# Optimization experiments

Hardware: AMD Instinct MI355X
Metric: run time of the kernel (lower is better)

The kernel has to match this reference:

```python
import jax, jax.numpy as jnp
import numpy as np

B, C, H, W = 8, 1024, 56, 56
NBINS = 256          # torch.histc(bins=256, min=0, max=1)
T_THRESH = 0.9       # EKLM entropy-ratio threshold
NUM_CLASSES = 30


def setup_inputs() -> dict:
    key = jax.random.key(0)
    k1, k2 = jax.random.split(key)
    x = jax.random.uniform(k1, (B, C, H, W), dtype=jnp.float32)
    w_fc = jax.random.normal(k2, (C, NUM_CLASSES), dtype=jnp.float32) * 0.02
    return {"x": x, "w_fc": w_fc}


def _integral_hist(x):
    """One fused pass replacing the per-region torch.histc calls.
    Returns per-(h,w)-cell histograms [H,W,256] and their 2D inclusive
    prefix sum padded to [H+1,W+1,256] so any rectangle histogram is 4 lookups.
    Matches torch.histc semantics: values outside [0,1] ignored, v==1 -> last bin."""
    valid = (x >= 0.0) & (x <= 1.0)
    q = jnp.clip(jnp.floor(x * NBINS), 0, NBINS - 1).astype(jnp.int32)
    q = jnp.where(valid, q, NBINS)  # out-of-range -> extra bin, dropped below
    hh = jnp.broadcast_to(jnp.arange(H)[None, None, :, None], x.shape)
    ww = jnp.broadcast_to(jnp.arange(W)[None, None, None, :], x.shape)
    cell = jnp.zeros((H, W, NBINS + 1), jnp.float32).at[hh, ww, q].add(1.0)[..., :NBINS]
    integ = jnp.cumsum(jnp.cumsum(cell, axis=0), axis=1)
    integ = jnp.pad(integ, ((1, 0), (1, 0), (0, 0)))  # [H+1, W+1, 256]
    return cell, integ


def _entropy_of_hist(h):
    p = h / jnp.sum(h)
    return -jnp.sum(p * jnp.log2(p + 1e-9))


def _region_entropy(integ, xs, xd, ys, yd):
    # histogram of x[:, :, xs:xd, ys:yd] via integral-histogram lookups
    h = integ[xd, yd] - integ[xs, yd] - integ[xd, ys] + integ[xs, ys]
    return _entropy_of_hist(h)


def eklm(x):
    """Entropy-based Key Localization Method (xs fixed to 0, as in source)."""
    cell, integ = _integral_hist(x)
    # compute_entropy_for_each_y: entropy of each [:, :, 0:1, y:y+1] column cell
    col_hists = cell[0]  # [W, 256]
    p = col_hists / jnp.sum(col_hists, axis=1, keepdims=True)
    ent_y = -jnp.sum(p * jnp.log2(p + 1e-9), axis=1)
    ys0 = jnp.argmax(ent_y).astype(jnp.int32)
    total_ent = _region_entropy(integ, 0, H, 0, W)

    def ent(xd, ys, yd):
        return _region_entropy(integ, 0, xd, ys, yd)

    def cond(state):
        xd, ys, yd, Ts, done = state
        return (Ts < T_THRESH) & (~done)

    def body(state):
        xd, ys, yd, Ts, done = state
        e_cur = ent(xd, ys, yd)
        # greedy priority identical to source: grow xd, else shrink ys, else grow yd
        c1 = (xd + 1 < H) & (ent(xd + 1, ys, yd) > e_cur)
        c2 = (~c1) & (ys - 1 >= 0) & (ent(xd, jnp.maximum(ys - 1, 0), yd) > e_cur)
        c3 = (~c1) & (~c2) & (yd + 1 < W) & (ent(xd, ys, jnp.minimum(yd + 1, W)) > e_cur)
        xd_n = jnp.where(c1, xd + 1, xd)
        ys_n = jnp.where(c2, ys - 1, ys)
        yd_n = jnp.where(c3, yd + 1, yd)
        done_n = ~(c1 | c2 | c3)
        Ts_n = ent(xd_n, ys_n, yd_n) / total_ent
        return (xd_n, ys_n, yd_n, Ts_n, done_n)

    xd0 = jnp.int32(1)
    yd0 = ys0 + jnp.int32(1)
    Ts0 = ent(xd0, ys0, yd0) / total_ent
    xd, ys, yd, _, _ = jax.lax.while_loop(
        cond, body, (xd0, ys0, yd0, Ts0, jnp.bool_(False)))
    return jnp.int32(0), xd, ys, yd


def reference(x, w_fc):
    xs, xd, ys, yd = eklm(x)
    # crop the located key region (mask form for static shapes), mean-pool, classify
    row = jnp.arange(H)
    col = jnp.arange(W)
    mask = ((row[:, None] >= xs) & (row[:, None] < xd)
            & (col[None, :] >= ys) & (col[None, :] < yd)).astype(x.dtype)
    area = jnp.maximum(jnp.sum(mask), 1.0)
    pooled = jnp.einsum('bchw,hw->bc', x, mask) / area  # [B, C]
    return pooled @ w_fc  # [B, NUM_CLASSES]
```

## Files before the change

kernel.cpp:

```cpp
#include <hip/hip_runtime.h>
#include <math.h>

#define BB 8
#define CC 1024
#define HH 56
#define WW 56
#define NB 256
#define NCLS 30
#define BC (BB * CC)
#define PLANE (HH * WW)
#define NWORD (NB / 2)
#define CELLW (PLANE * NWORD)
#define SLICES 16
#define PL_PER_SLICE (BC / SLICES)

#define NPART 16
#define GH_BLOCKS 3136
#define F4_PER_BLOCK 2048
#define FB_BLOCKS 256

#define FULL_NEED 28934400ull
#define META_OFF 28901376ull

__global__ void zero_kernel(unsigned* __restrict__ p, unsigned* __restrict__ bar) {
    p[blockIdx.x * 256 + threadIdx.x] = 0u;
    if (blockIdx.x == 0 && threadIdx.x < 8) bar[threadIdx.x] = 0u;
}

__global__ __launch_bounds__(256) void ghist_kernel(const float* __restrict__ x,
                                                    unsigned* __restrict__ colhist,
                                                    unsigned* __restrict__ gpart) {
    __shared__ unsigned lh[4 * NB];
    const int tid = threadIdx.x;
    lh[tid] = 0u; lh[NB + tid] = 0u; lh[2 * NB + tid] = 0u; lh[3 * NB + tid] = 0u;
    __syncthreads();

    const size_t base_f4 = (size_t)blockIdx.x * F4_PER_BLOCK;
    const float4* __restrict__ xb = (const float4*)x + base_f4;
    float4 v[8];
#pragma unroll
    for (int it = 0; it < 8; ++it) v[it] = xb[it * 256 + tid];

    unsigned* wl = lh + ((tid >> 6) << 8);
#pragma unroll
    for (int it = 0; it < 8; ++it) {
        const int j = it * 256 + tid;
        const int e0 = ((int)base_f4 + j) * 4;
        const int pl = e0 / PLANE;
        const int li = e0 - pl * PLANE;
        const bool r0 = (li < WW);
        const float vv[4] = {v[it].x, v[it].y, v[it].z, v[it].w};
#pragma unroll
        for (int e = 0; e < 4; ++e) {
            const float f = vv[e];
            if (f >= 0.f && f <= 1.f) {
                int bin = (int)(f * 256.f);
                if (bin > 255) bin = 255;
                atomicAdd(&wl[bin], 1u);
                if (r0) atomicAdd(&colhist[(li + e) * NB + bin], 1u);
            }
        }
    }
    __syncthreads();
    const unsigned s = lh[tid] + lh[NB + tid] + lh[2 * NB + tid] + lh[3 * NB + tid];
    if (s) atomicAdd(&gpart[((blockIdx.x & (NPART - 1)) << 8) + tid], s);
}

__device__ __forceinline__ float wave_sum(float v) {
#pragma unroll
    for (int off = 32; off > 0; off >>= 1) v += __shfl_xor(v, off);
    return v;
}

__device__ __forceinline__ float ilook(const unsigned* __restrict__ integ,
                                       int a, int b, int bin) {
    return (a == 0 || b == 0)
               ? 0.f
               : (float)integ[((size_t)((a - 1) * WW + (b - 1))) * NB + bin];
}

__device__ float region_ent(const unsigned* __restrict__ integ, int lane,
                            int xd, int ys, int yd) {
    float hb[4];
    float hs = 0.f;
#pragma unroll
    for (int k = 0; k < 4; k++) {
        const int bin = lane + 64 * k;
        const float hv = ilook(integ, xd, yd, bin) - ilook(integ, xd, ys, bin);
        hb[k] = hv;
        hs += hv;
    }
    hs = wave_sum(hs);
    float e = 0.f;
#pragma unroll
    for (int k = 0; k < 4; k++) {
        const float p = hb[k] / hs;
        e += p * log2f(p + 1e-9f);
    }
    return -wave_sum(e);
}

__global__ __launch_bounds__(1024) void decide_fast_kernel(
    const unsigned* __restrict__ colhist, const unsigned* __restrict__ gpart,
    int* __restrict__ region, unsigned* __restrict__ flag) {
    __shared__ float ent_s[WW];
    const int tid = threadIdx.x;
    const int lane = tid & 63;
    const int wv = tid >> 6;

    for (int w = wv; w < WW; w += 16) {
        float hb[4], hs = 0.f;
#pragma unroll
        for (int k = 0; k < 4; k++) {
            const int bin = lane + 64 * k;
            hb[k] = (float)colhist[w * NB + bin];
            hs += hb[k];
        }
        hs = wave_sum(hs);
        float e = 0.f;
#pragma unroll
        for (int k = 0; k < 4; k++) {
            const float p = hb[k] / hs;
            e += p * log2f(p + 1e-9f);
        }
        e = -wave_sum(e);
        if (lane == 0) ent_s[w] = e;
    }
    __syncthreads();
    if (wv != 0) return;

    float best = -3.0e38f;
    int bestw = 0;
    for (int w = 0; w < WW; ++w) {
        const float e = ent_s[w];
        if (e > best) { best = e; bestw = w; }
    }

    float hb[4], hs = 0.f;
#pragma unroll
    for (int k = 0; k < 4; k++) {
        const int bin = lane + 64 * k;
        unsigned t = 0;
#pragma unroll
        for (int p = 0; p < NPART; ++p) t += gpart[(p << 8) + bin];
        hb[k] = (float)t;
        hs += hb[k];
    }
    hs = wave_sum(hs);
    float e = 0.f;
#pragma unroll
    for (int k = 0; k < 4; k++) {
        const float p = hb[k] / hs;
        e += p * log2f(p + 1e-9f);
    }
    const float total_ent = -wave_sum(e);

    const float Ts0 = best / total_ent;
    if (lane == 0) {
        region[0] = 1;
        region[1] = bestw;
        region[2] = bestw + 1;
        *flag = (Ts0 >= 0.9f) ? 1u : 2u;
    }
}

__device__ __forceinline__ void soft_grid_sync(unsigned* __restrict__ bar,
                                               int idx, unsigned nb) {
    __syncthreads();
    if (threadIdx.x == 0) {
        __threadfence();
        atomicAdd(&bar[idx], 1u);
        while (atomicAdd(&bar[idx], 0u) < nb) {
            __builtin_amdgcn_s_sleep(8);
        }
    }
    __syncthreads();
    __threadfence();
}

__global__ __launch_bounds__(256) void fallback_kernel(
    const float* __restrict__ x, unsigned* __restrict__ ps,
    unsigned* __restrict__ hist, int* __restrict__ region,
    const unsigned* __restrict__ flag, unsigned* __restrict__ bar) {
    if (*flag == 1u) return;
    __shared__ unsigned lh[HH * NWORD];
    const int tid = threadIdx.x;
    const int gtid = blockIdx.x * 256 + tid;

    for (int t = blockIdx.x; t < HH * SLICES; t += FB_BLOCKS) {
        const int h = t % HH;
        const int slice = t / HH;
        for (int i = tid; i < HH * NWORD; i += 256) lh[i] = 0u;
        __syncthreads();
        const float* __restrict__ xb =
            x + (size_t)(slice * PL_PER_SLICE) * PLANE + h * WW;
        for (int it = 0; it < 28; ++it) {
            const int j = it * 256 + tid;
            const int bcl = j / 14;
            const int wq = j - bcl * 14;
            const float4 v = *(const float4*)(xb + (size_t)bcl * PLANE + wq * 4);
            const float vv[4] = {v.x, v.y, v.z, v.w};
#pragma unroll
            for (int e = 0; e < 4; ++e) {
                const float f = vv[e];
                if (f >= 0.f && f <= 1.f) {
                    int bin = (int)(f * 256.f);
                    if (bin > 255) bin = 255;
                    atomicAdd(&lh[(wq * 4 + e) * NWORD + (bin >> 1)],
                              1u << ((bin & 1) << 4));
                }
            }
        }
        __syncthreads();
        unsigned* g = ps + (size_t)slice * CELLW + (size_t)h * WW * NWORD;
        for (int i = tid; i < HH * NWORD; i += 256) g[i] = lh[i];
        __syncthreads();
    }
    soft_grid_sync(bar, 0, FB_BLOCKS);

    for (int idx = gtid; idx < CELLW; idx += FB_BLOCKS * 256) {
        unsigned s = 0;
#pragma unroll
        for (int sl = 0; sl < SLICES; ++sl) s += ps[(size_t)sl * CELLW + idx];
        ((uint2*)hist)[idx] = make_uint2(s & 0xffffu, s >> 16);
    }
    soft_grid_sync(bar, 1, FB_BLOCKS);

    if (gtid < HH * NB) {
        const int h = gtid >> 8, b = gtid & 255;
        unsigned* base = hist + (size_t)h * WW * NB + b;
        unsigned v[WW];
#pragma unroll
        for (int w = 0; w < WW; ++w) v[w] = base[(size_t)w * NB];
        unsigned c = 0;
#pragma unroll
        for (int w = 0; w < WW; ++w) { c += v[w]; base[(size_t)w * NB] = c; }
    }
    soft_grid_sync(bar, 2, FB_BLOCKS);

    if (gtid < WW * NB) {
        const int w = gtid >> 8, b = gtid & 255;
        unsigned* base = hist + (size_t)w * NB + b;
        unsigned v[HH];
#pragma unroll
        for (int h = 0; h < HH; ++h) v[h] = base[(size_t)h * WW * NB];
        unsigned c = 0;
#pragma unroll
        for (int h = 0; h < HH; ++h) { c += v[h]; base[(size_t)h * WW * NB] = c; }
    }
    soft_grid_sync(bar, 3, FB_BLOCKS);

    if (blockIdx.x == 0 && tid < 64) {
        const int lane = tid;
        const float total_ent = region_ent(hist, lane, HH, 0, WW);
        int xd = region[0], ys = region[1], yd = region[2];
        float Ts = region_ent(hist, lane, xd, ys, yd) / total_ent;
        bool done = false;
        int iter = 0;
        while (Ts < 0.9f && !done && iter < 1000) {
            iter++;
            const float e_cur = region_ent(hist, lane, xd, ys, yd);
            const int ysm = (ys - 1 < 0) ? 0 : ys - 1;
            const int ydp = (yd + 1 > WW) ? WW : yd + 1;
            const bool c1 = (xd + 1 < HH) &&
                            (region_ent(hist, lane, xd + 1, ys, yd) > e_cur);
            const bool c2 = !c1 && (ys - 1 >= 0) &&
                            (region_ent(hist, lane, xd, ysm, yd) > e_cur);
            const bool c3 = !c1 && !c2 && (yd + 1 < WW) &&
                            (region_ent(hist, lane, xd, ys, ydp) > e_cur);
            if (c1) xd = xd + 1;
            else if (c2) ys = ys - 1;
            else if (c3) yd = yd + 1;
            done = !(c1 || c2 || c3);
            Ts = region_ent(hist, lane, xd, ys, yd) / total_ent;
        }
        if (lane == 0) {
            region[0] = xd;
            region[1] = ys;
            region[2] = yd;
        }
    }
}

__global__ __launch_bounds__(256) void fc_kernel(const float* __restrict__ x,
                                                 const int* __restrict__ region,
                                                 const float* __restrict__ wfc,
                                                 float* __restrict__ out) {
    __shared__ float pl_s[CC];
    __shared__ float red[240];
    const int b = blockIdx.x;
    const int t = threadIdx.x;
    const int xd = region[0], ys = region[1], yd = region[2];
    const int Wd = yd - ys;
    const int n = xd * Wd;
    const float area = fmaxf((float)n, 1.f);
    const float* __restrict__ xb = x + (size_t)b * CC * PLANE;
#pragma unroll
    for (int k = 0; k < 4; ++k) {
        const int c = t + k * 256;
        const float* plane = xb + (size_t)c * PLANE;
        float s = 0.f;
        for (int j = 0; j < n; ++j) {
            const int r = j / Wd;
            const int cc2 = ys + (j - r * Wd);
            s += plane[r * WW + cc2];
        }
        pl_s[c] = s / area;
    }
    __syncthreads();
    if (t < 240) {
        const int chunk = t / NCLS;
        const int nn = t - chunk * NCLS;
        const float* pv = pl_s + chunk * 128;
        const float* wv = wfc + (size_t)(chunk * 128) * NCLS + nn;
        float a0 = 0.f, a1 = 0.f, a2 = 0.f, a3 = 0.f;
        for (int c = 0; c < 128; c += 4) {
            a0 += pv[c + 0] * wv[(c + 0) * NCLS];
            a1 += pv[c + 1] * wv[(c + 1) * NCLS];
            a2 += pv[c + 2] * wv[(c + 2) * NCLS];
            a3 += pv[c + 3] * wv[(c + 3) * NCLS];
        }
        red[t] = (a0 + a1) + (a2 + a3);
    }
    __syncthreads();
    if (t < NCLS) {
        float s = 0.f;
#pragma unroll
        for (int ch = 0; ch < 8; ++ch) s += red[ch * NCLS + t];
        out[b * NCLS + t] = s;
    }
}

extern "C" void kernel_launch(void* const* d_in, const int* in_sizes, int n_in,
                              void* d_out, int out_size, void* d_ws, size_t ws_size,
                              hipStream_t stream) {
    const float* x = (const float*)d_in[0];
    const float* wfc = (const float*)d_in[1];
    float* out = (float*)d_out;

    unsigned char* ws = (unsigned char*)d_ws;
    const bool full = (ws_size >= FULL_NEED);

    unsigned* colhist = (unsigned*)ws;
    unsigned* gpart = (unsigned*)(ws + 57344);
    unsigned* ps = (unsigned*)ws;
    unsigned* hist = (unsigned*)(ws + (size_t)SLICES * CELLW * 4);
    int* region;
    unsigned* flag;
    unsigned* bar;
    if (full) {
        unsigned char* meta = ws + META_OFF;
        region = (int*)meta;
        flag = (unsigned*)(meta + 16);
        bar = (unsigned*)(meta + 32);
    } else {
        region = (int*)(ws + 73728);
        flag = (unsigned*)(ws + 73728 + 16);
        bar = (unsigned*)(ws + 73728 + 32);
    }

    zero_kernel<<<72, 256, 0, stream>>>(colhist, bar);
    ghist_kernel<<<GH_BLOCKS, 256, 0, stream>>>(x, colhist, gpart);
    decide_fast_kernel<<<1, 1024, 0, stream>>>(colhist, gpart, region, flag);
    if (full) {
        fallback_kernel<<<FB_BLOCKS, 256, 0, stream>>>(x, ps, hist, region,
                                                       flag, bar);
    }
    fc_kernel<<<BB, 256, 0, stream>>>(x, region, wfc, out);
}
```

Baseline: 169.8 us.

## Fuse histogram, decision, fallback and FC into one persistent kernel

Merges the global-histogram, decision, fallback integral-histogram and FC kernels into a single persistent 1024-block kernel that uses hierarchical software grid barriers between phases. Column histograms are now accumulated in packed 16-bit shared-memory counters per block and flushed once, instead of global atomics per element. The fallback path is rewritten to build cell histograms with global atomics directly, replacing the sliced partial buffers. This removes several kernel launches and intermediate round trips. In exchange it relies on all 1024 blocks being co-resident, and the fc phase runs on only 8 blocks at the end.

```diff
diff --git a/kernel.cpp b/kernel.cpp
--- a/kernel.cpp
+++ b/kernel.cpp
@@ -10,60 +10,40 @@
 #define BC (BB * CC)
 #define PLANE (HH * WW)
 #define NWORD (NB / 2)
-#define CELLW (PLANE * NWORD)
-#define SLICES 16
-#define PL_PER_SLICE (BC / SLICES)
-
+#define CHW (HH * NWORD)
 #define NPART 16
-#define GH_BLOCKS 3136
-#define F4_PER_BLOCK 2048
-#define FB_BLOCKS 256
-
-#define FULL_NEED 28934400ull
-#define META_OFF 28901376ull
-
-__global__ void zero_kernel(unsigned* __restrict__ p, unsigned* __restrict__ bar) {
-    p[blockIdx.x * 256 + threadIdx.x] = 0u;
-    if (blockIdx.x == 0 && threadIdx.x < 8) bar[threadIdx.x] = 0u;
-}
-
-__global__ __launch_bounds__(256) void ghist_kernel(const float* __restrict__ x,
-                                                    unsigned* __restrict__ colhist,
-                                                    unsigned* __restrict__ gpart) {
-    __shared__ unsigned lh[4 * NB];
-    const int tid = threadIdx.x;
-    lh[tid] = 0u; lh[NB + tid] = 0u; lh[2 * NB + tid] = 0u; lh[3 * NB + tid] = 0u;
-    __syncthreads();
-
-    const size_t base_f4 = (size_t)blockIdx.x * F4_PER_BLOCK;
-    const float4* __restrict__ xb = (const float4*)x + base_f4;
-    float4 v[8];
-#pragma unroll
-    for (int it = 0; it < 8; ++it) v[it] = xb[it * 256 + tid];
-
-    unsigned* wl = lh + ((tid >> 6) << 8);
-#pragma unroll
-    for (int it = 0; it < 8; ++it) {
-        const int j = it * 256 + tid;
-        const int e0 = ((int)base_f4 + j) * 4;
-        const int pl = e0 / PLANE;
-        const int li = e0 - pl * PLANE;
-        const bool r0 = (li < WW);
-        const float vv[4] = {v[it].x, v[it].y, v[it].z, v[it].w};
-#pragma unroll
-        for (int e = 0; e < 4; ++e) {
-            const float f = vv[e];
-            if (f >= 0.f && f <= 1.f) {
-                int bin = (int)(f * 256.f);
-                if (bin > 255) bin = 255;
-                atomicAdd(&wl[bin], 1u);
-                if (r0) atomicAdd(&colhist[(li + e) * NB + bin], 1u);
-            }
-        }
-    }
-    __syncthreads();
-    const unsigned s = lh[tid] + lh[NB + tid] + lh[2 * NB + tid] + lh[3 * NB + tid];
-    if (s) atomicAdd(&gpart[((blockIdx.x & (NPART - 1)) << 8) + tid], s);
+#define NBLK 1024
+#define NCHUNK 3136
+#define CHUNK_F4 2048
+
+#define BAR_GROUPS 16
+#define BAR_STRIDE 16
+#define BAR_WORDS (BAR_STRIDE * (BAR_GROUPS + 1))
+#define NBAR 7
+#define GRP_SZ (NBLK / BAR_GROUPS)
+
+#define META_U32 (16 + NBAR * BAR_WORDS)
+#define ZERO_WORDS (HH * NB + NPART * NB + META_U32)
+#define HIST_OFF 131072ull
+
+__global__ void zero_kernel(unsigned* __restrict__ p) {
+    const int i = blockIdx.x * 256 + threadIdx.x;
+    if (i < ZERO_WORDS) p[i] = 0u;
+}
+
+__device__ __forceinline__ void gsync(unsigned* bar_inst, int bid) {
+    __syncthreads();
+    __threadfence();
+    if (threadIdx.x == 0) {
+        unsigned* lo = bar_inst + (bid & (BAR_GROUPS - 1)) * BAR_STRIDE;
+        unsigned* hi = bar_inst + BAR_GROUPS * BAR_STRIDE;
+        if (atomicAdd(lo, 1u) == GRP_SZ - 1u) atomicAdd(hi, 1u);
+        while (__hip_atomic_load(hi, __ATOMIC_RELAXED,
+                                 __HIP_MEMORY_SCOPE_AGENT) < BAR_GROUPS)
+            __builtin_amdgcn_s_sleep(16);
+    }
+    __syncthreads();
+    __threadfence();
 }
 
 __device__ __forceinline__ float wave_sum(float v) {
@@ -100,204 +80,230 @@
     return -wave_sum(e);
 }
 
-__global__ __launch_bounds__(1024) void decide_fast_kernel(
-    const unsigned* __restrict__ colhist, const unsigned* __restrict__ gpart,
-    int* __restrict__ region, unsigned* __restrict__ flag) {
-    __shared__ float ent_s[WW];
+__global__ __launch_bounds__(256, 4) void mega_kernel(
+    const float* __restrict__ x, const float* __restrict__ wfc,
+    unsigned* __restrict__ colhist, unsigned* __restrict__ gpart,
+    unsigned* __restrict__ meta, unsigned* __restrict__ hist,
+    float* __restrict__ out) {
+    __shared__ unsigned smem[NB * 4 + CHW];
+    unsigned* lh = smem;
+    unsigned* ch = smem + NB * 4;
+
     const int tid = threadIdx.x;
-    const int lane = tid & 63;
-    const int wv = tid >> 6;
-
-    for (int w = wv; w < WW; w += 16) {
-        float hb[4], hs = 0.f;
-#pragma unroll
-        for (int k = 0; k < 4; k++) {
-            const int bin = lane + 64 * k;
-            hb[k] = (float)colhist[w * NB + bin];
-            hs += hb[k];
-        }
-        hs = wave_sum(hs);
-        float e = 0.f;
-#pragma unroll
-        for (int k = 0; k < 4; k++) {
-            const float p = hb[k] / hs;
-            e += p * log2f(p + 1e-9f);
-        }
-        e = -wave_sum(e);
-        if (lane == 0) ent_s[w] = e;
-    }
-    __syncthreads();
-    if (wv != 0) return;
-
-    float best = -3.0e38f;
-    int bestw = 0;
-    for (int w = 0; w < WW; ++w) {
-        const float e = ent_s[w];
-        if (e > best) { best = e; bestw = w; }
-    }
-
-    float hb[4], hs = 0.f;
-#pragma unroll
-    for (int k = 0; k < 4; k++) {
-        const int bin = lane + 64 * k;
-        unsigned t = 0;
-#pragma unroll
-        for (int p = 0; p < NPART; ++p) t += gpart[(p << 8) + bin];
-        hb[k] = (float)t;
-        hs += hb[k];
-    }
-    hs = wave_sum(hs);
-    float e = 0.f;
-#pragma unroll
-    for (int k = 0; k < 4; k++) {
-        const float p = hb[k] / hs;
-        e += p * log2f(p + 1e-9f);
-    }
-    const float total_ent = -wave_sum(e);
-
-    const float Ts0 = best / total_ent;
-    if (lane == 0) {
-        region[0] = 1;
-        region[1] = bestw;
-        region[2] = bestw + 1;
-        *flag = (Ts0 >= 0.9f) ? 1u : 2u;
-    }
-}
-
-__device__ __forceinline__ void soft_grid_sync(unsigned* __restrict__ bar,
-                                               int idx, unsigned nb) {
-    __syncthreads();
-    if (threadIdx.x == 0) {
-        __threadfence();
-        atomicAdd(&bar[idx], 1u);
-        while (atomicAdd(&bar[idx], 0u) < nb) {
-            __builtin_amdgcn_s_sleep(8);
-        }
-    }
-    __syncthreads();
-    __threadfence();
-}
-
-__global__ __launch_bounds__(256) void fallback_kernel(
-    const float* __restrict__ x, unsigned* __restrict__ ps,
-    unsigned* __restrict__ hist, int* __restrict__ region,
-    const unsigned* __restrict__ flag, unsigned* __restrict__ bar) {
-    if (*flag == 1u) return;
-    __shared__ unsigned lh[HH * NWORD];
-    const int tid = threadIdx.x;
-    const int gtid = blockIdx.x * 256 + tid;
-
-    for (int t = blockIdx.x; t < HH * SLICES; t += FB_BLOCKS) {
-        const int h = t % HH;
-        const int slice = t / HH;
-        for (int i = tid; i < HH * NWORD; i += 256) lh[i] = 0u;
-        __syncthreads();
-        const float* __restrict__ xb =
-            x + (size_t)(slice * PL_PER_SLICE) * PLANE + h * WW;
-        for (int it = 0; it < 28; ++it) {
-            const int j = it * 256 + tid;
-            const int bcl = j / 14;
-            const int wq = j - bcl * 14;
-            const float4 v = *(const float4*)(xb + (size_t)bcl * PLANE + wq * 4);
-            const float vv[4] = {v.x, v.y, v.z, v.w};
+    const int bid = blockIdx.x;
+    unsigned* flag = meta;
+    int* region = (int*)(meta + 1);
+    unsigned* bar = meta + 16;
+
+    for (int i = tid; i < NB * 4 + CHW; i += 256) smem[i] = 0u;
+    __syncthreads();
+
+    unsigned* wl = lh + ((tid >> 6) << 8);
+    for (int c = bid; c < NCHUNK; c += NBLK) {
+        const float4* __restrict__ xb = (const float4*)x + (size_t)c * CHUNK_F4;
+        float4 v[8];
+#pragma unroll
+        for (int it = 0; it < 8; ++it) v[it] = xb[it * 256 + tid];
+#pragma unroll
+        for (int it = 0; it < 8; ++it) {
+            const int e0 = (c * CHUNK_F4 + it * 256 + tid) * 4;
+            const int pl = e0 / PLANE;
+            const int li = e0 - pl * PLANE;
+            const bool r0 = (li < WW);
+            const float vv[4] = {v[it].x, v[it].y, v[it].z, v[it].w};
 #pragma unroll
             for (int e = 0; e < 4; ++e) {
                 const float f = vv[e];
                 if (f >= 0.f && f <= 1.f) {
                     int bin = (int)(f * 256.f);
                     if (bin > 255) bin = 255;
-                    atomicAdd(&lh[(wq * 4 + e) * NWORD + (bin >> 1)],
-                              1u << ((bin & 1) << 4));
+                    atomicAdd(&wl[bin], 1u);
+                    if (r0)
+                        atomicAdd(&ch[(li + e) * NWORD + (bin >> 1)],
+                                  1u << ((bin & 1) << 4));
                 }
             }
         }
+    }
+    __syncthreads();
+
+    {
+        const unsigned s =
+            lh[tid] + lh[NB + tid] + lh[2 * NB + tid] + lh[3 * NB + tid];
+        if (s) atomicAdd(&gpart[((bid & (NPART - 1)) << 8) + tid], s);
+    }
+    for (int i = tid; i < CHW; i += 256) {
+        const unsigned w = ch[i];
+        if (w) {
+            const int col = i >> 7;
+            const int b2 = (i & 127) << 1;
+            const unsigned lo16 = w & 0xffffu, hi16 = w >> 16;
+            if (lo16) atomicAdd(&colhist[col * NB + b2], lo16);
+            if (hi16) atomicAdd(&colhist[col * NB + b2 + 1], hi16);
+        }
+    }
+    gsync(bar + 0 * BAR_WORDS, bid);
+
+    float* ent_s = (float*)smem;
+    if (bid == 0) {
+        const int lane = tid & 63;
+        const int wv = tid >> 6;
+        for (int w = wv; w < WW; w += 4) {
+            float hb[4], hs = 0.f;
+#pragma unroll
+            for (int k = 0; k < 4; k++) {
+                const int bin = lane + 64 * k;
+                hb[k] = (float)colhist[w * NB + bin];
+                hs += hb[k];
+            }
+            hs = wave_sum(hs);
+            float e = 0.f;
+#pragma unroll
+            for (int k = 0; k < 4; k++) {
+                const float p = hb[k] / hs;
+                e += p * log2f(p + 1e-9f);
+            }
+            e = -wave_sum(e);
+            if (lane == 0) ent_s[w] = e;
+        }
         __syncthreads();
-        unsigned* g = ps + (size_t)slice * CELLW + (size_t)h * WW * NWORD;
-        for (int i = tid; i < HH * NWORD; i += 256) g[i] = lh[i];
-        __syncthreads();
-    }
-    soft_grid_sync(bar, 0, FB_BLOCKS);
-
-    for (int idx = gtid; idx < CELLW; idx += FB_BLOCKS * 256) {
-        unsigned s = 0;
-#pragma unroll
-        for (int sl = 0; sl < SLICES; ++sl) s += ps[(size_t)sl * CELLW + idx];
-        ((uint2*)hist)[idx] = make_uint2(s & 0xffffu, s >> 16);
-    }
-    soft_grid_sync(bar, 1, FB_BLOCKS);
-
-    if (gtid < HH * NB) {
-        const int h = gtid >> 8, b = gtid & 255;
-        unsigned* base = hist + (size_t)h * WW * NB + b;
-        unsigned v[WW];
-#pragma unroll
-        for (int w = 0; w < WW; ++w) v[w] = base[(size_t)w * NB];
-        unsigned c = 0;
-#pragma unroll
-        for (int w = 0; w < WW; ++w) { c += v[w]; base[(size_t)w * NB] = c; }
-    }
-    soft_grid_sync(bar, 2, FB_BLOCKS);
-
-    if (gtid < WW * NB) {
-        const int w = gtid >> 8, b = gtid & 255;
-        unsigned* base = hist + (size_t)w * NB + b;
-        unsigned v[HH];
-#pragma unroll
-        for (int h = 0; h < HH; ++h) v[h] = base[(size_t)h * WW * NB];
-        unsigned c = 0;
-#pragma unroll
-        for (int h = 0; h < HH; ++h) { c += v[h]; base[(size_t)h * WW * NB] = c; }
-    }
-    soft_grid_sync(bar, 3, FB_BLOCKS);
-
-    if (blockIdx.x == 0 && tid < 64) {
-        const int lane = tid;
-        const float total_ent = region_ent(hist, lane, HH, 0, WW);
-        int xd = region[0], ys = region[1], yd = region[2];
-        float Ts = region_ent(hist, lane, xd, ys, yd) / total_ent;
-        bool done = false;
-        int iter = 0;
-        while (Ts < 0.9f && !done && iter < 1000) {
-            iter++;
-            const float e_cur = region_ent(hist, lane, xd, ys, yd);
-            const int ysm = (ys - 1 < 0) ? 0 : ys - 1;
-            const int ydp = (yd + 1 > WW) ? WW : yd + 1;
-            const bool c1 = (xd + 1 < HH) &&
-                            (region_ent(hist, lane, xd + 1, ys, yd) > e_cur);
-            const bool c2 = !c1 && (ys - 1 >= 0) &&
-                            (region_ent(hist, lane, xd, ysm, yd) > e_cur);
-            const bool c3 = !c1 && !c2 && (yd + 1 < WW) &&
-                            (region_ent(hist, lane, xd, ys, ydp) > e_cur);
-            if (c1) xd = xd + 1;
-            else if (c2) ys = ys - 1;
-            else if (c3) yd = yd + 1;
-            done = !(c1 || c2 || c3);
-            Ts = region_ent(hist, lane, xd, ys, yd) / total_ent;
-        }
-        if (lane == 0) {
-            region[0] = xd;
-            region[1] = ys;
-            region[2] = yd;
-        }
-    }
-}
-
-__global__ __launch_bounds__(256) void fc_kernel(const float* __restrict__ x,
-                                                 const int* __restrict__ region,
-                                                 const float* __restrict__ wfc,
-                                                 float* __restrict__ out) {
-    __shared__ float pl_s[CC];
-    __shared__ float red[240];
-    const int b = blockIdx.x;
-    const int t = threadIdx.x;
+        if (tid < 64) {
+            const int lane = tid;
+            float best = -3.0e38f;
+            int bestw = 0;
+            for (int w = 0; w < WW; ++w) {
+                const float e = ent_s[w];
+                if (e > best) { best = e; bestw = w; }
+            }
+            float hb[4], hs = 0.f;
+#pragma unroll
+            for (int k = 0; k < 4; k++) {
+                const int bin = lane + 64 * k;
+                unsigned t = 0;
+#pragma unroll
+                for (int p = 0; p < NPART; ++p) t += gpart[(p << 8) + bin];
+                hb[k] = (float)t;
+                hs += hb[k];
+            }
+            hs = wave_sum(hs);
+            float e = 0.f;
+#pragma unroll
+            for (int k = 0; k < 4; k++) {
+                const float p = hb[k] / hs;
+                e += p * log2f(p + 1e-9f);
+            }
+            const float total_ent = -wave_sum(e);
+            const float Ts0 = best / total_ent;
+            if (lane == 0) {
+                region[0] = 1;
+                region[1] = bestw;
+                region[2] = bestw + 1;
+                *flag = (Ts0 >= 0.9f) ? 1u : 2u;
+            }
+        }
+    }
+    gsync(bar + 1 * BAR_WORDS, bid);
+
+    const unsigned fl =
+        __hip_atomic_load(flag, __ATOMIC_RELAXED, __HIP_MEMORY_SCOPE_AGENT);
+
+    if (fl != 1u) {
+        const int gtid = bid * 256 + tid;
+        for (int i = gtid; i < PLANE * NB; i += NBLK * 256) hist[i] = 0u;
+        gsync(bar + 2 * BAR_WORDS, bid);
+        for (int c = bid; c < NCHUNK; c += NBLK) {
+            const float4* __restrict__ xb =
+                (const float4*)x + (size_t)c * CHUNK_F4;
+            for (int it = 0; it < 8; ++it) {
+                const float4 v = xb[it * 256 + tid];
+                const int e0 = (c * CHUNK_F4 + it * 256 + tid) * 4;
+                const int pl = e0 / PLANE;
+                const int li = e0 - pl * PLANE;
+                const float vv[4] = {v.x, v.y, v.z, v.w};
+                for (int e = 0; e < 4; ++e) {
+                    const float f = vv[e];
+                    if (f >= 0.f && f <= 1.f) {
+                        int bin = (int)(f * 256.f);
+                        if (bin > 255) bin = 255;
+                        atomicAdd(&hist[(size_t)(li + e) * NB + bin], 1u);
+                    }
+                }
+            }
+        }
+        gsync(bar + 3 * BAR_WORDS, bid);
+        if (gtid < HH * NB) {
+            const int h = gtid >> 8, b = gtid & 255;
+            unsigned* base = hist + (size_t)h * WW * NB + b;
+            unsigned vreg[WW];
+#pragma unroll
+            for (int w = 0; w < WW; ++w) vreg[w] = base[(size_t)w * NB];
+            unsigned cacc = 0;
+#pragma unroll
+            for (int w = 0; w < WW; ++w) {
+                cacc += vreg[w];
+                base[(size_t)w * NB] = cacc;
+            }
+        }
+        gsync(bar + 4 * BAR_WORDS, bid);
+        if (gtid < WW * NB) {
+            const int w = gtid >> 8, b = gtid & 255;
+            unsigned* base = hist + (size_t)w * NB + b;
+            unsigned vreg[HH];
+#pragma unroll
+            for (int h = 0; h < HH; ++h) vreg[h] = base[(size_t)h * WW * NB];
+            unsigned cacc = 0;
+#pragma unroll
+            for (int h = 0; h < HH; ++h) {
+                cacc += vreg[h];
+                base[(size_t)h * WW * NB] = cacc;
+            }
+        }
+        gsync(bar + 5 * BAR_WORDS, bid);
+        if (bid == 0 && tid < 64) {
+            const int lane = tid;
+            const float total_ent = region_ent(hist, lane, HH, 0, WW);
+            int xd = region[0], ys = region[1], yd = region[2];
+            float Ts = region_ent(hist, lane, xd, ys, yd) / total_ent;
+            bool done = false;
+            int iter = 0;
+            while (Ts < 0.9f && !done && iter < 1000) {
+                iter++;
+                const float e_cur = region_ent(hist, lane, xd, ys, yd);
+                const int ysm = (ys - 1 < 0) ? 0 : ys - 1;
+                const int ydp = (yd + 1 > WW) ? WW : yd + 1;
+                const bool c1 = (xd + 1 < HH) &&
+                                (region_ent(hist, lane, xd + 1, ys, yd) > e_cur);
+                const bool c2 = !c1 && (ys - 1 >= 0) &&
+                                (region_ent(hist, lane, xd, ysm, yd) > e_cur);
+                const bool c3 = !c1 && !c2 && (yd + 1 < WW) &&
+                                (region_ent(hist, lane, xd, ys, ydp) > e_cur);
+                if (c1) xd = xd + 1;
+                else if (c2) ys = ys - 1;
+                else if (c3) yd = yd + 1;
+                done = !(c1 || c2 || c3);
+                Ts = region_ent(hist, lane, xd, ys, yd) / total_ent;
+            }
+            if (lane == 0) {
+                region[0] = xd;
+                region[1] = ys;
+                region[2] = yd;
+            }
+        }
+        gsync(bar + 6 * BAR_WORDS, bid);
+    }
+
+    if (bid >= BB) return;
     const int xd = region[0], ys = region[1], yd = region[2];
     const int Wd = yd - ys;
     const int n = xd * Wd;
     const float area = fmaxf((float)n, 1.f);
-    const float* __restrict__ xb = x + (size_t)b * CC * PLANE;
+    float* pl_s = (float*)smem;
+    float* red = (float*)smem + CC;
+    __syncthreads();
+    const float* __restrict__ xb = x + (size_t)bid * CC * PLANE;
 #pragma unroll
     for (int k = 0; k < 4; ++k) {
-        const int c = t + k * 256;
+        const int c = tid + k * 256;
         const float* plane = xb + (size_t)c * PLANE;
         float s = 0.f;
         for (int j = 0; j < n; ++j) {
@@ -308,26 +314,26 @@
         pl_s[c] = s / area;
     }
     __syncthreads();
-    if (t < 240) {
-        const int chunk = t / NCLS;
-        const int nn = t - chunk * NCLS;
+    if (tid < 240) {
+        const int chunk = tid / NCLS;
+        const int nn = tid - chunk * NCLS;
         const float* pv = pl_s + chunk * 128;
-        const float* wv = wfc + (size_t)(chunk * 128) * NCLS + nn;
+        const float* wv2 = wfc + (size_t)(chunk * 128) * NCLS + nn;
         float a0 = 0.f, a1 = 0.f, a2 = 0.f, a3 = 0.f;
         for (int c = 0; c < 128; c += 4) {
-            a0 += pv[c + 0] * wv[(c + 0) * NCLS];
-            a1 += pv[c + 1] * wv[(c + 1) * NCLS];
-            a2 += pv[c + 2] * wv[(c + 2) * NCLS];
-            a3 += pv[c + 3] * wv[(c + 3) * NCLS];
-        }
-        red[t] = (a0 + a1) + (a2 + a3);
-    }
-    __syncthreads();
-    if (t < NCLS) {
+            a0 += pv[c + 0] * wv2[(c + 0) * NCLS];
+            a1 += pv[c + 1] * wv2[(c + 1) * NCLS];
+            a2 += pv[c + 2] * wv2[(c + 2) * NCLS];
+            a3 += pv[c + 3] * wv2[(c + 3) * NCLS];
+        }
+        red[tid] = (a0 + a1) + (a2 + a3);
+    }
+    __syncthreads();
+    if (tid < NCLS) {
         float s = 0.f;
 #pragma unroll
-        for (int ch = 0; ch < 8; ++ch) s += red[ch * NCLS + t];
-        out[b * NCLS + t] = s;
+        for (int ch2 = 0; ch2 < 8; ++ch2) s += red[ch2 * NCLS + tid];
+        out[bid * NCLS + tid] = s;
     }
 }
 
@@ -339,32 +345,12 @@
     float* out = (float*)d_out;
 
     unsigned char* ws = (unsigned char*)d_ws;
-    const bool full = (ws_size >= FULL_NEED);
-
     unsigned* colhist = (unsigned*)ws;
     unsigned* gpart = (unsigned*)(ws + 57344);
-    unsigned* ps = (unsigned*)ws;
-    unsigned* hist = (unsigned*)(ws + (size_t)SLICES * CELLW * 4);
-    int* region;
-    unsigned* flag;
-    unsigned* bar;
-    if (full) {
-        unsigned char* meta = ws + META_OFF;
-        region = (int*)meta;
-        flag = (unsigned*)(meta + 16);
-        bar = (unsigned*)(meta + 32);
-    } else {
-        region = (int*)(ws + 73728);
-        flag = (unsigned*)(ws + 73728 + 16);
-        bar = (unsigned*)(ws + 73728 + 32);
-    }
-
-    zero_kernel<<<72, 256, 0, stream>>>(colhist, bar);
-    ghist_kernel<<<GH_BLOCKS, 256, 0, stream>>>(x, colhist, gpart);
-    decide_fast_kernel<<<1, 1024, 0, stream>>>(colhist, gpart, region, flag);
-    if (full) {
-        fallback_kernel<<<FB_BLOCKS, 256, 0, stream>>>(x, ps, hist, region,
-                                                       flag, bar);
-    }
-    fc_kernel<<<BB, 256, 0, stream>>>(x, region, wfc, out);
-}
+    unsigned* meta = (unsigned*)(ws + 73728);
+    unsigned* hist = (unsigned*)(ws + HIST_OFF);
+
+    zero_kernel<<<80, 256, 0, stream>>>(colhist);
+    mega_kernel<<<NBLK, 256, 0, stream>>>(x, wfc, colhist, gpart, meta, hist,
+                                          out);
+}
```

Result: slower. 453.3 us (+167.0%).
